# Performance work log

Hardware: AMD Instinct MI355X
Metric: run time of the kernel (lower is better)

The kernel has to match this reference:

```python
import jax, jax.numpy as jnp
import numpy as np

NEG_BIG = -9.0e15  # matches -9000000000000000.0 in the torch source


def setup_inputs() -> dict:
    key = jax.random.key(0)
    k1, k2 = jax.random.split(key)
    N, D, L = 8192, 128, 2
    features = jax.random.normal(k1, (N, D), dtype=jnp.float32)
    adj_lst = jax.random.randint(k2, (L, N, N), 0, 2, dtype=jnp.int32)
    return {"features": features, "adj_lst": adj_lst}


def reference(features, adj_lst):
    # features: [N, D] float; adj_lst: [L, N, N] int (0/1)
    n_node = features.shape[0]
    for i in range(adj_lst.shape[0]):  # small fixed number of propagation steps
        adj = adj_lst[i]
        mask = adj > 0
        # raw_weight = ones -> masked logits are 1.0 on edges, -9e15 elsewhere
        logits = jnp.where(mask, jnp.float32(1.0), jnp.float32(NEG_BIG))
        attention = jax.nn.softmax(logits, axis=1)          # [N, N] row-stochastic
        prop_fea = attention @ features                     # [N, D] neighbor mean
        adj_num = jnp.sum(adj, axis=1)                      # degree per node
        adj_mask = (adj_num > 0).astype(features.dtype)[:, None]  # [N, 1]
        features = adj_mask * prop_fea + (1.0 - adj_mask) * features
    return features
```

## Files before the change

### kernel.cpp

```cpp
#include <hip/hip_runtime.h>
#include <hip/hip_bf16.h>

typedef __bf16 bf16x8 __attribute__((ext_vector_type(8)));
typedef float f32x4 __attribute__((ext_vector_type(4)));
typedef float f32x16 __attribute__((ext_vector_type(16)));
typedef int int4v __attribute__((ext_vector_type(4)));
typedef unsigned int uint4v __attribute__((ext_vector_type(4)));
typedef unsigned short u16x8 __attribute__((ext_vector_type(8)));

#define N_NODES 8192
#define D_FEAT 128

__device__ __forceinline__ bf16x8 unpack_byte(unsigned dword, int sh) {
  unsigned P = ((dword >> sh) & 0xFFu) * 0x8001u;
  uint4v c;
  c[0] = (P & 0x10001u) * 0x3F80u;
  c[1] = ((P >> 2) & 0x10001u) * 0x3F80u;
  c[2] = ((P >> 4) & 0x10001u) * 0x3F80u;
  c[3] = ((P >> 6) & 0x10001u) * 0x3F80u;
  return __builtin_bit_cast(bf16x8, c);
}

__device__ __forceinline__ void bpk32_store(const float* __restrict__ src,
                                            unsigned short* __restrict__ Bpk,
                                            int W) {
  const int kk = W >> 8;
  const int ng = (W >> 6) & 3;
  const int l = W & 63;
  const int d = ng * 32 + (l & 31);
  const int p0 = kk * 16 + (l >> 5) * 8;
  const int n0 = (p0 >> 8) * 256 + ((p0 >> 3) & 7) * 32 + ((p0 >> 6) & 3);
  u16x8 pk;
#pragma unroll
  for (int e = 0; e < 8; ++e) {
    __bf16 v = (__bf16)src[(long)(n0 + 4 * e) * D_FEAT + d];
    pk[e] = __builtin_bit_cast(unsigned short, v);
  }
  *(u16x8*)(Bpk + (long)W * 8) = pk;
}

__global__ __launch_bounds__(256) void pack_all_kernel(
    const int* __restrict__ adj, unsigned long long* __restrict__ bits64,
    int* __restrict__ deg, const float* __restrict__ fsrc,
    unsigned short* __restrict__ Bpk) {
  const int bx = blockIdx.x;
  const int t = threadIdx.x;

  if (bx < 512) {
    bpk32_store(fsrc, Bpk, bx * 256 + t);
    return;
  }

  const int row = bx - 512;
  const int w = t >> 6;
  const int lane = t & 63;
  const int4v* p = (const int4v*)(adj + ((long)row << 13));
  int4v v[8];
#pragma unroll
  for (int j = 0; j < 8; ++j) v[j] = p[j * 256 + t];

  unsigned long long* brow = bits64 + ((long)row << 7);
  int cnt = 0;
#pragma unroll
  for (int j = 0; j < 8; ++j) {
    unsigned long long b0 = __ballot(v[j][0] != 0);
    unsigned long long b1 = __ballot(v[j][1] != 0);
    unsigned long long b2 = __ballot(v[j][2] != 0);
    unsigned long long b3 = __ballot(v[j][3] != 0);
    cnt += __popcll(b0) + __popcll(b1) + __popcll(b2) + __popcll(b3);
    unsigned long long bsel = b0;
    if (lane == 1) bsel = b1;
    if (lane == 2) bsel = b2;
    if (lane == 3) bsel = b3;
    if (lane < 4) brow[16 * j + 4 * w + lane] = bsel;
  }
  __shared__ int red[4];
  if (lane == 0) red[w] = cnt;
  __syncthreads();
  if (t == 0) deg[row] = red[0] + red[1] + red[2] + red[3];
}

__global__ __launch_bounds__(256) void bpk_build32_kernel(
    const float* __restrict__ src, unsigned short* __restrict__ Bpk) {
  bpk32_store(src, Bpk, blockIdx.x * 256 + threadIdx.x);
}

__device__ __forceinline__ void layer_body32(
    int rowblk, int nthalf,
    const unsigned* __restrict__ bits, const int* __restrict__ deg,
    const unsigned short* __restrict__ Bpk,
    const float* fin, float* fout,
    f32x4 (*red)[2][2][4][64]) {
  const int tid = threadIdx.x;
  const int lane = tid & 63;
  const int w = tid >> 6;
  const int ntl = w & 1;
  const int kh = w >> 1;
  const int l31 = lane & 31;
  const int lh = lane >> 5;
  const int m0 = rowblk * 64;
  const int ng = nthalf * 2 + ntl;
  const int shA = lh * 8;
  const int shB = shA + 16;

  const uint4v* ap0 = (const uint4v*)(bits + ((long)(m0 + l31) << 8)) + kh * 16;
  const uint4v* ap1 =
      (const uint4v*)(bits + ((long)(m0 + 32 + l31) << 8)) + kh * 16;
  const bf16x8* bp = (const bf16x8*)Bpk + ((long)kh << 15) + ng * 64 + lane;

  f32x16 acc0 = {0.f, 0.f, 0.f, 0.f, 0.f, 0.f, 0.f, 0.f,
                 0.f, 0.f, 0.f, 0.f, 0.f, 0.f, 0.f, 0.f};
  f32x16 acc1 = {0.f, 0.f, 0.f, 0.f, 0.f, 0.f, 0.f, 0.f,
                 0.f, 0.f, 0.f, 0.f, 0.f, 0.f, 0.f, 0.f};

#pragma unroll 2
  for (int kg = 0; kg < 16; ++kg) {
    uint4v a0 = ap0[kg];
    uint4v a1 = ap1[kg];
#pragma unroll
    for (int s = 0; s < 8; ++s) {
      bf16x8 bv = *bp;
      bp += 256;
      const int sh = (s & 1) ? shB : shA;
      acc0 = __builtin_amdgcn_mfma_f32_32x32x16_bf16(
          unpack_byte(a0[s >> 1], sh), bv, acc0, 0, 0, 0);
      acc1 = __builtin_amdgcn_mfma_f32_32x32x16_bf16(
          unpack_byte(a1[s >> 1], sh), bv, acc1, 0, 0, 0);
    }
  }

  if (kh) {
#define STORE_CHUNK(c)                                                       \
  red[kh - 1][ntl][0][c][lane] = __builtin_shufflevector(                    \
      acc0, acc0, 4 * (c), 4 * (c) + 1, 4 * (c) + 2, 4 * (c) + 3);           \
  red[kh - 1][ntl][1][c][lane] = __builtin_shufflevector(                    \
      acc1, acc1, 4 * (c), 4 * (c) + 1, 4 * (c) + 2, 4 * (c) + 3);
    STORE_CHUNK(0)
    STORE_CHUNK(1)
    STORE_CHUNK(2)
    STORE_CHUNK(3)
#undef STORE_CHUNK
  }
  __syncthreads();
  if (kh) return;

#pragma unroll
  for (int q = 0; q < 3; ++q) {
#pragma unroll
    for (int c = 0; c < 4; ++c) {
      f32x4 r0 = red[q][ntl][0][c][lane];
      f32x4 r1 = red[q][ntl][1][c][lane];
#pragma unroll
      for (int k = 0; k < 4; ++k) {
        acc0[4 * c + k] += r0[k];
        acc1[4 * c + k] += r1[k];
      }
    }
  }

#pragma unroll
  for (int mt = 0; mt < 2; ++mt) {
#pragma unroll
    for (int r = 0; r < 16; ++r) {
      const int row = m0 + mt * 32 + (r & 3) + 8 * (r >> 2) + 4 * lh;
      const int dg = deg[row];
      const float a = mt ? acc1[r] : acc0[r];
      const long off = (long)row * D_FEAT + ng * 32 + l31;
      fout[off] = dg > 0 ? a * (1.0f / (float)dg) : fin[off];
    }
  }
}

__global__ __launch_bounds__(512, 2) void layer32_kernel(
    const unsigned* __restrict__ bits, const int* __restrict__ deg,
    const unsigned short* __restrict__ Bpk, const float* fin, float* fout) {
  __shared__ __align__(16) f32x4 red[3][2][2][4][64];
  layer_body32(blockIdx.x >> 1, blockIdx.x & 1, bits, deg, Bpk, fin, fout,
               red);
}

__global__ __launch_bounds__(256) void transpose_cast_kernel(
    const float* __restrict__ src, unsigned short* __restrict__ dst) {
  __shared__ float tile[64][129];
  const int t = threadIdx.x;
  const int nbase = blockIdx.x * 64;
#pragma unroll
  for (int i = 0; i < 32; ++i) {
    int idx = t + i * 256;
    int nl = idx >> 7;
    int d = idx & 127;
    tile[nl][d] = src[(long)(nbase + nl) * D_FEAT + d];
  }
  __syncthreads();
#pragma unroll
  for (int i = 0; i < 32; ++i) {
    int idx = t + i * 256;
    int d = idx >> 6;
    int nl = idx & 63;
    __bf16 b = (__bf16)tile[nl][d];
    dst[(long)d * N_NODES + nbase + nl] = __builtin_bit_cast(unsigned short, b);
  }
}

__global__ __launch_bounds__(512) void layer_kernel_direct(
    const int* __restrict__ adj, const unsigned short* __restrict__ BT,
    const float* __restrict__ fin, float* __restrict__ fout) {
  const int tid = threadIdx.x;
  const int lane = tid & 63;
  const int w = tid >> 6;
  const int m0 = blockIdx.x * 32 + (w >> 2) * 16;
  const int n0 = (w & 3) * 32;
  const int lr = lane & 15;
  const int kc = lane >> 4;

  const int4v* ap = (const int4v*)(adj + (long)(m0 + lr) * N_NODES + kc * 8);
  const bf16x8* bp0 = (const bf16x8*)(BT + (long)(n0 + lr) * N_NODES + kc * 8);
  const bf16x8* bp1 =
      (const bf16x8*)(BT + (long)(n0 + 16 + lr) * N_NODES + kc * 8);

  f32x4 acc0 = {0.f, 0.f, 0.f, 0.f};
  f32x4 acc1 = {0.f, 0.f, 0.f, 0.f};
  int degv = 0;

#pragma unroll 4
  for (int k = 0; k < N_NODES; k += 32) {
    int4v alo = ap[0];
    int4v ahi = ap[1];
    bf16x8 b0 = bp0[0];
    bf16x8 b1 = bp1[0];
    ap += 8;
    bp0 += 4;
    bp1 += 4;
    unsigned short u[8];
    u[0] = alo[0] ? 0x3F80 : 0;
    u[1] = alo[1] ? 0x3F80 : 0;
    u[2] = alo[2] ? 0x3F80 : 0;
    u[3] = alo[3] ? 0x3F80 : 0;
    u[4] = ahi[0] ? 0x3F80 : 0;
    u[5] = ahi[1] ? 0x3F80 : 0;
    u[6] = ahi[2] ? 0x3F80 : 0;
    u[7] = ahi[3] ? 0x3F80 : 0;
    degv += alo[0] + alo[1] + alo[2] + alo[3] + ahi[0] + ahi[1] + ahi[2] +
            ahi[3];
    bf16x8 a;
    memcpy(&a, u, 16);
    acc0 = __builtin_amdgcn_mfma_f32_16x16x32_bf16(a, b0, acc0, 0, 0, 0);
    acc1 = __builtin_amdgcn_mfma_f32_16x16x32_bf16(a, b1, acc1, 0, 0, 0);
  }

  degv += __shfl_xor(degv, 16);
  degv += __shfl_xor(degv, 32);
  int dgv[4];
#pragma unroll
  for (int j = 0; j < 4; ++j) dgv[j] = __shfl(degv, kc * 4 + j);

#pragma unroll
  for (int t = 0; t < 2; ++t) {
    const f32x4 acc = t ? acc1 : acc0;
    const int col = n0 + t * 16 + lr;
#pragma unroll
    for (int j = 0; j < 4; ++j) {
      const long off = (long)(m0 + kc * 4 + j) * D_FEAT + col;
      fout[off] = dgv[j] > 0 ? acc[j] * (1.0f / (float)dgv[j]) : fin[off];
    }
  }
}

extern "C" void kernel_launch(void* const* d_in, const int* in_sizes, int n_in,
                              void* d_out, int out_size, void* d_ws,
                              size_t ws_size, hipStream_t stream) {
  const float* features = (const float*)d_in[0];
  const int* adj = (const int*)d_in[1];
  float* out = (float*)d_out;
  const long NN = (long)N_NODES * N_NODES;

  const size_t BITS_BYTES = 2ul * N_NODES * 128 * 8;
  const size_t BPK_BYTES = (size_t)D_FEAT * N_NODES * 2;
  const size_t NEED = BITS_BYTES + 65536 + BPK_BYTES;

  if (ws_size >= NEED) {
    unsigned long long* bits64 = (unsigned long long*)d_ws;
    int* degw = (int*)((char*)d_ws + BITS_BYTES);
    unsigned short* Bpk = (unsigned short*)((char*)d_ws + BITS_BYTES + 65536);
    const unsigned* bits32 = (const unsigned*)d_ws;

    pack_all_kernel<<<2 * N_NODES + 512, 256, 0, stream>>>(adj, bits64, degw,
                                                           features, Bpk);
    layer32_kernel<<<256, 512, 0, stream>>>(bits32, degw, Bpk, features, out);
    bpk_build32_kernel<<<512, 256, 0, stream>>>(out, Bpk);
    layer32_kernel<<<256, 512, 0, stream>>>(bits32 + (size_t)N_NODES * 256,
                                            degw + N_NODES, Bpk, out, out);
  } else {
    unsigned short* BTw = (unsigned short*)d_ws;
    transpose_cast_kernel<<<N_NODES / 64, 256, 0, stream>>>(features, BTw);
    layer_kernel_direct<<<N_NODES / 32, 512, 0, stream>>>(adj, BTw, features,
                                                          out);
    transpose_cast_kernel<<<N_NODES / 64, 256, 0, stream>>>(out, BTw);
    layer_kernel_direct<<<N_NODES / 32, 512, 0, stream>>>(adj + NN, BTw, out,
                                                          out);
  }
}
```

Baseline: 175.5 us.

## Persistent adjacency packing with nontemporal loads and 2x2 MFMA tiles per wave

The packing kernel now launches 2048 row blocks that each loop over 8 rows, and it reads the adjacency matrix with nontemporal loads. This cuts block launch overhead and avoids polluting the cache with the large int32 adjacency stream. The layer kernel now has each wave compute a 2x2 set of 32x32 MFMA tiles over one-eighth of K, so each B fragment is reused across two A tiles and each unpacked A across two B tiles. The cross-wave K reduction becomes a two-stage tree through LDS, which adds registers (four accumulators), extra syncs and more LDS.

```diff
diff --git a/kernel.cpp b/kernel.cpp
--- a/kernel.cpp
+++ b/kernel.cpp
@@ -51,38 +51,64 @@
     return;
   }
 
-  const int row = bx - 512;
+  const int bxp = bx - 512;
   const int w = t >> 6;
   const int lane = t & 63;
-  const int4v* p = (const int4v*)(adj + ((long)row << 13));
-  int4v v[8];
-#pragma unroll
-  for (int j = 0; j < 8; ++j) v[j] = p[j * 256 + t];
-
-  unsigned long long* brow = bits64 + ((long)row << 7);
-  int cnt = 0;
-#pragma unroll
-  for (int j = 0; j < 8; ++j) {
-    unsigned long long b0 = __ballot(v[j][0] != 0);
-    unsigned long long b1 = __ballot(v[j][1] != 0);
-    unsigned long long b2 = __ballot(v[j][2] != 0);
-    unsigned long long b3 = __ballot(v[j][3] != 0);
-    cnt += __popcll(b0) + __popcll(b1) + __popcll(b2) + __popcll(b3);
-    unsigned long long bsel = b0;
-    if (lane == 1) bsel = b1;
-    if (lane == 2) bsel = b2;
-    if (lane == 3) bsel = b3;
-    if (lane < 4) brow[16 * j + 4 * w + lane] = bsel;
-  }
-  __shared__ int red[4];
-  if (lane == 0) red[w] = cnt;
-  __syncthreads();
-  if (t == 0) deg[row] = red[0] + red[1] + red[2] + red[3];
+  __shared__ int red[2][4];
+
+  for (int it = 0; it < 8; ++it) {
+    const int row = bxp + it * 2048;
+    const int4v* p = (const int4v*)(adj + ((long)row << 13));
+    int4v v[8];
+#pragma unroll
+    for (int j = 0; j < 8; ++j)
+      v[j] = __builtin_nontemporal_load(p + j * 256 + t);
+
+    unsigned long long* brow = bits64 + ((long)row << 7);
+    int cnt = 0;
+#pragma unroll
+    for (int j = 0; j < 8; ++j) {
+      unsigned long long b0 = __ballot(v[j][0] != 0);
+      unsigned long long b1 = __ballot(v[j][1] != 0);
+      unsigned long long b2 = __ballot(v[j][2] != 0);
+      unsigned long long b3 = __ballot(v[j][3] != 0);
+      cnt += __popcll(b0) + __popcll(b1) + __popcll(b2) + __popcll(b3);
+      unsigned long long bsel = b0;
+      if (lane == 1) bsel = b1;
+      if (lane == 2) bsel = b2;
+      if (lane == 3) bsel = b3;
+      if (lane < 4) brow[16 * j + 4 * w + lane] = bsel;
+    }
+    if (lane == 0) red[it & 1][w] = cnt;
+    __syncthreads();
+    if (t == 0)
+      deg[row] =
+          red[it & 1][0] + red[it & 1][1] + red[it & 1][2] + red[it & 1][3];
+  }
 }
 
 __global__ __launch_bounds__(256) void bpk_build32_kernel(
     const float* __restrict__ src, unsigned short* __restrict__ Bpk) {
   bpk32_store(src, Bpk, blockIdx.x * 256 + threadIdx.x);
+}
+
+__device__ __forceinline__ void st_acc(f32x4 (*red)[16][64], int slot, int A,
+                                       int lane, f32x16 v) {
+  red[slot][A * 4 + 0][lane] = __builtin_shufflevector(v, v, 0, 1, 2, 3);
+  red[slot][A * 4 + 1][lane] = __builtin_shufflevector(v, v, 4, 5, 6, 7);
+  red[slot][A * 4 + 2][lane] = __builtin_shufflevector(v, v, 8, 9, 10, 11);
+  red[slot][A * 4 + 3][lane] = __builtin_shufflevector(v, v, 12, 13, 14, 15);
+}
+__device__ __forceinline__ void ld_acc(f32x4 (*red)[16][64], int slot, int A,
+                                       int lane, f32x16* v) {
+#pragma unroll
+  for (int c = 0; c < 4; ++c) {
+    f32x4 r = red[slot][A * 4 + c][lane];
+    (*v)[4 * c + 0] += r[0];
+    (*v)[4 * c + 1] += r[1];
+    (*v)[4 * c + 2] += r[2];
+    (*v)[4 * c + 3] += r[3];
+  }
 }
 
 __device__ __forceinline__ void layer_body32(
@@ -90,83 +116,90 @@
     const unsigned* __restrict__ bits, const int* __restrict__ deg,
     const unsigned short* __restrict__ Bpk,
     const float* fin, float* fout,
-    f32x4 (*red)[2][2][4][64]) {
+    f32x4 (*red)[16][64]) {
   const int tid = threadIdx.x;
   const int lane = tid & 63;
   const int w = tid >> 6;
-  const int ntl = w & 1;
-  const int kh = w >> 1;
   const int l31 = lane & 31;
   const int lh = lane >> 5;
   const int m0 = rowblk * 64;
-  const int ng = nthalf * 2 + ntl;
+  const int ng0 = nthalf * 2;
   const int shA = lh * 8;
-  const int shB = shA + 16;
-
-  const uint4v* ap0 = (const uint4v*)(bits + ((long)(m0 + l31) << 8)) + kh * 16;
+
+  const uint4v* ap0 = (const uint4v*)(bits + ((long)(m0 + l31) << 8)) + w * 8;
   const uint4v* ap1 =
-      (const uint4v*)(bits + ((long)(m0 + 32 + l31) << 8)) + kh * 16;
-  const bf16x8* bp = (const bf16x8*)Bpk + ((long)kh << 15) + ng * 64 + lane;
-
-  f32x16 acc0 = {0.f, 0.f, 0.f, 0.f, 0.f, 0.f, 0.f, 0.f,
-                 0.f, 0.f, 0.f, 0.f, 0.f, 0.f, 0.f, 0.f};
-  f32x16 acc1 = {0.f, 0.f, 0.f, 0.f, 0.f, 0.f, 0.f, 0.f,
-                 0.f, 0.f, 0.f, 0.f, 0.f, 0.f, 0.f, 0.f};
+      (const uint4v*)(bits + ((long)(m0 + 32 + l31) << 8)) + w * 8;
+  const bf16x8* bp = (const bf16x8*)Bpk + ((long)w << 14) + ng0 * 64 + lane;
+
+  f32x16 acc00 = {0.f, 0.f, 0.f, 0.f, 0.f, 0.f, 0.f, 0.f,
+                  0.f, 0.f, 0.f, 0.f, 0.f, 0.f, 0.f, 0.f};
+  f32x16 acc01 = acc00, acc10 = acc00, acc11 = acc00;
 
 #pragma unroll 2
-  for (int kg = 0; kg < 16; ++kg) {
+  for (int kg = 0; kg < 8; ++kg) {
     uint4v a0 = ap0[kg];
     uint4v a1 = ap1[kg];
 #pragma unroll
     for (int s = 0; s < 8; ++s) {
-      bf16x8 bv = *bp;
+      bf16x8 bv0 = bp[0];
+      bf16x8 bv1 = bp[64];
       bp += 256;
-      const int sh = (s & 1) ? shB : shA;
-      acc0 = __builtin_amdgcn_mfma_f32_32x32x16_bf16(
-          unpack_byte(a0[s >> 1], sh), bv, acc0, 0, 0, 0);
-      acc1 = __builtin_amdgcn_mfma_f32_32x32x16_bf16(
-          unpack_byte(a1[s >> 1], sh), bv, acc1, 0, 0, 0);
+      const int sh = shA + (s & 1) * 16;
+      bf16x8 af0 = unpack_byte(a0[s >> 1], sh);
+      bf16x8 af1 = unpack_byte(a1[s >> 1], sh);
+      acc00 = __builtin_amdgcn_mfma_f32_32x32x16_bf16(af0, bv0, acc00, 0, 0, 0);
+      acc10 = __builtin_amdgcn_mfma_f32_32x32x16_bf16(af1, bv0, acc10, 0, 0, 0);
+      acc01 = __builtin_amdgcn_mfma_f32_32x32x16_bf16(af0, bv1, acc01, 0, 0, 0);
+      acc11 = __builtin_amdgcn_mfma_f32_32x32x16_bf16(af1, bv1, acc11, 0, 0, 0);
     }
   }
 
-  if (kh) {
-#define STORE_CHUNK(c)                                                       \
-  red[kh - 1][ntl][0][c][lane] = __builtin_shufflevector(                    \
-      acc0, acc0, 4 * (c), 4 * (c) + 1, 4 * (c) + 2, 4 * (c) + 3);           \
-  red[kh - 1][ntl][1][c][lane] = __builtin_shufflevector(                    \
-      acc1, acc1, 4 * (c), 4 * (c) + 1, 4 * (c) + 2, 4 * (c) + 3);
-    STORE_CHUNK(0)
-    STORE_CHUNK(1)
-    STORE_CHUNK(2)
-    STORE_CHUNK(3)
-#undef STORE_CHUNK
+  if (w >= 4) {
+    st_acc(red, w - 4, 0, lane, acc00);
+    st_acc(red, w - 4, 1, lane, acc01);
+    st_acc(red, w - 4, 2, lane, acc10);
+    st_acc(red, w - 4, 3, lane, acc11);
   }
   __syncthreads();
-  if (kh) return;
-
-#pragma unroll
-  for (int q = 0; q < 3; ++q) {
-#pragma unroll
-    for (int c = 0; c < 4; ++c) {
-      f32x4 r0 = red[q][ntl][0][c][lane];
-      f32x4 r1 = red[q][ntl][1][c][lane];
-#pragma unroll
-      for (int k = 0; k < 4; ++k) {
-        acc0[4 * c + k] += r0[k];
-        acc1[4 * c + k] += r1[k];
+  if (w < 4) {
+    ld_acc(red, w, 0, lane, &acc00);
+    ld_acc(red, w, 1, lane, &acc01);
+    ld_acc(red, w, 2, lane, &acc10);
+    ld_acc(red, w, 3, lane, &acc11);
+  }
+  __syncthreads();
+  if (w >= 1 && w < 4) {
+    st_acc(red, w, 0, lane, acc00);
+    st_acc(red, w, 1, lane, acc01);
+    st_acc(red, w, 2, lane, acc10);
+    st_acc(red, w, 3, lane, acc11);
+  }
+  __syncthreads();
+  if (w != 0) return;
+#pragma unroll
+  for (int q = 1; q < 4; ++q) {
+    ld_acc(red, q, 0, lane, &acc00);
+    ld_acc(red, q, 1, lane, &acc01);
+    ld_acc(red, q, 2, lane, &acc10);
+    ld_acc(red, q, 3, lane, &acc11);
+  }
+
+#pragma unroll
+  for (int mt = 0; mt < 2; ++mt) {
+#pragma unroll
+    for (int nn = 0; nn < 2; ++nn) {
+#pragma unroll
+      for (int r = 0; r < 16; ++r) {
+        const int row = m0 + mt * 32 + (r & 3) + 8 * (r >> 2) + 4 * lh;
+        const int dg = deg[row];
+        float a;
+        if (mt == 0 && nn == 0) a = acc00[r];
+        else if (mt == 0 && nn == 1) a = acc01[r];
+        else if (mt == 1 && nn == 0) a = acc10[r];
+        else a = acc11[r];
+        const long off = (long)row * D_FEAT + (ng0 + nn) * 32 + l31;
+        fout[off] = dg > 0 ? a * (1.0f / (float)dg) : fin[off];
       }
-    }
-  }
-
-#pragma unroll
-  for (int mt = 0; mt < 2; ++mt) {
-#pragma unroll
-    for (int r = 0; r < 16; ++r) {
-      const int row = m0 + mt * 32 + (r & 3) + 8 * (r >> 2) + 4 * lh;
-      const int dg = deg[row];
-      const float a = mt ? acc1[r] : acc0[r];
-      const long off = (long)row * D_FEAT + ng * 32 + l31;
-      fout[off] = dg > 0 ? a * (1.0f / (float)dg) : fin[off];
     }
   }
 }
@@ -174,7 +207,7 @@
 __global__ __launch_bounds__(512, 2) void layer32_kernel(
     const unsigned* __restrict__ bits, const int* __restrict__ deg,
     const unsigned short* __restrict__ Bpk, const float* fin, float* fout) {
-  __shared__ __align__(16) f32x4 red[3][2][2][4][64];
+  __shared__ __align__(16) f32x4 red[4][16][64];
   layer_body32(blockIdx.x >> 1, blockIdx.x & 1, bits, deg, Bpk, fin, fout,
                red);
 }
@@ -284,8 +317,8 @@
     unsigned short* Bpk = (unsigned short*)((char*)d_ws + BITS_BYTES + 65536);
     const unsigned* bits32 = (const unsigned*)d_ws;
 
-    pack_all_kernel<<<2 * N_NODES + 512, 256, 0, stream>>>(adj, bits64, degw,
-                                                           features, Bpk);
+    pack_all_kernel<<<2048 + 512, 256, 0, stream>>>(adj, bits64, degw,
+                                                    features, Bpk);
     layer32_kernel<<<256, 512, 0, stream>>>(bits32, degw, Bpk, features, out);
     bpk_build32_kernel<<<512, 256, 0, stream>>>(out, Bpk);
     layer32_kernel<<<256, 512, 0, stream>>>(bits32 + (size_t)N_NODES * 256,
```

New measurement: 183.1 us. +4.4%, slower.

## Fuse adjacency bit-packing and degree counting into the layer GEMM kernel

Applied to the files above, without the earlier changes.

Removes the separate pack kernel that converted the whole int32 adjacency into a global bitmask and degree array. Each layer kernel now streams its own 32 adjacency rows, ballots them into a double-buffered shared-memory bitmask and counts degrees. The bf16 MFMA GEMM on the previous chunk runs while the next chunks are prefetched, so the adjacency read overlaps with compute. The cost is one block per 32 rows, only 256 blocks, with a barrier per chunk. Bandwidth saturation now depends on the register prefetch depth rather than on massive block parallelism.

```diff
diff --git a/kernel.cpp b/kernel.cpp
--- a/kernel.cpp
+++ b/kernel.cpp
@@ -10,6 +10,7 @@
 
 #define N_NODES 8192
 #define D_FEAT 128
+
 
 __device__ __forceinline__ bf16x8 unpack_byte(unsigned dword, int sh) {
   unsigned P = ((dword >> sh) & 0xFFu) * 0x8001u;
@@ -39,144 +40,144 @@
   *(u16x8*)(Bpk + (long)W * 8) = pk;
 }
 
-__global__ __launch_bounds__(256) void pack_all_kernel(
-    const int* __restrict__ adj, unsigned long long* __restrict__ bits64,
-    int* __restrict__ deg, const float* __restrict__ fsrc,
-    unsigned short* __restrict__ Bpk) {
-  const int bx = blockIdx.x;
-  const int t = threadIdx.x;
-
-  if (bx < 512) {
-    bpk32_store(fsrc, Bpk, bx * 256 + t);
-    return;
-  }
-
-  const int row = bx - 512;
-  const int w = t >> 6;
-  const int lane = t & 63;
-  const int4v* p = (const int4v*)(adj + ((long)row << 13));
-  int4v v[8];
-#pragma unroll
-  for (int j = 0; j < 8; ++j) v[j] = p[j * 256 + t];
-
-  unsigned long long* brow = bits64 + ((long)row << 7);
-  int cnt = 0;
-#pragma unroll
-  for (int j = 0; j < 8; ++j) {
-    unsigned long long b0 = __ballot(v[j][0] != 0);
-    unsigned long long b1 = __ballot(v[j][1] != 0);
-    unsigned long long b2 = __ballot(v[j][2] != 0);
-    unsigned long long b3 = __ballot(v[j][3] != 0);
-    cnt += __popcll(b0) + __popcll(b1) + __popcll(b2) + __popcll(b3);
-    unsigned long long bsel = b0;
-    if (lane == 1) bsel = b1;
-    if (lane == 2) bsel = b2;
-    if (lane == 3) bsel = b3;
-    if (lane < 4) brow[16 * j + 4 * w + lane] = bsel;
-  }
-  __shared__ int red[4];
-  if (lane == 0) red[w] = cnt;
-  __syncthreads();
-  if (t == 0) deg[row] = red[0] + red[1] + red[2] + red[3];
-}
-
 __global__ __launch_bounds__(256) void bpk_build32_kernel(
     const float* __restrict__ src, unsigned short* __restrict__ Bpk) {
   bpk32_store(src, Bpk, blockIdx.x * 256 + threadIdx.x);
 }
 
-__device__ __forceinline__ void layer_body32(
-    int rowblk, int nthalf,
-    const unsigned* __restrict__ bits, const int* __restrict__ deg,
-    const unsigned short* __restrict__ Bpk,
-    const float* fin, float* fout,
-    f32x4 (*red)[2][2][4][64]) {
+__global__ __launch_bounds__(512, 2) void fused_layer_kernel(
+    const int* __restrict__ adj, const unsigned short* __restrict__ Bpk,
+    const float* __restrict__ fin, float* __restrict__ fout) {
+  __shared__ unsigned bitsL[2][320];
+  __shared__ int degL[32];
+  __shared__ __align__(16) f32x4 red[4][4][64];
+
   const int tid = threadIdx.x;
   const int lane = tid & 63;
   const int w = tid >> 6;
-  const int ntl = w & 1;
-  const int kh = w >> 1;
+  const int ng = w & 3;
+  const int kh2 = w >> 2;
   const int l31 = lane & 31;
   const int lh = lane >> 5;
-  const int m0 = rowblk * 64;
-  const int ng = nthalf * 2 + ntl;
-  const int shA = lh * 8;
-  const int shB = shA + 16;
-
-  const uint4v* ap0 = (const uint4v*)(bits + ((long)(m0 + l31) << 8)) + kh * 16;
-  const uint4v* ap1 =
-      (const uint4v*)(bits + ((long)(m0 + 32 + l31) << 8)) + kh * 16;
-  const bf16x8* bp = (const bf16x8*)Bpk + ((long)kh << 15) + ng * 64 + lane;
-
-  f32x16 acc0 = {0.f, 0.f, 0.f, 0.f, 0.f, 0.f, 0.f, 0.f,
-                 0.f, 0.f, 0.f, 0.f, 0.f, 0.f, 0.f, 0.f};
-  f32x16 acc1 = {0.f, 0.f, 0.f, 0.f, 0.f, 0.f, 0.f, 0.f,
-                 0.f, 0.f, 0.f, 0.f, 0.f, 0.f, 0.f, 0.f};
-
-#pragma unroll 2
-  for (int kg = 0; kg < 16; ++kg) {
-    uint4v a0 = ap0[kg];
-    uint4v a1 = ap1[kg];
-#pragma unroll
-    for (int s = 0; s < 8; ++s) {
-      bf16x8 bv = *bp;
-      bp += 256;
-      const int sh = (s & 1) ? shB : shA;
-      acc0 = __builtin_amdgcn_mfma_f32_32x32x16_bf16(
-          unpack_byte(a0[s >> 1], sh), bv, acc0, 0, 0, 0);
-      acc1 = __builtin_amdgcn_mfma_f32_32x32x16_bf16(
-          unpack_byte(a1[s >> 1], sh), bv, acc1, 0, 0, 0);
-    }
-  }
-
-  if (kh) {
-#define STORE_CHUNK(c)                                                       \
-  red[kh - 1][ntl][0][c][lane] = __builtin_shufflevector(                    \
-      acc0, acc0, 4 * (c), 4 * (c) + 1, 4 * (c) + 2, 4 * (c) + 3);           \
-  red[kh - 1][ntl][1][c][lane] = __builtin_shufflevector(                    \
-      acc1, acc1, 4 * (c), 4 * (c) + 1, 4 * (c) + 2, 4 * (c) + 3);
-    STORE_CHUNK(0)
-    STORE_CHUNK(1)
-    STORE_CHUNK(2)
-    STORE_CHUNK(3)
-#undef STORE_CHUNK
-  }
+  const int lh8 = lh * 8;
+  const int m0 = blockIdx.x * 32;
+
+  const int4v* aB0 = (const int4v*)(adj + ((long)(m0 + w) << 13)) + lane;
+  const int4v* aB1 = (const int4v*)(adj + ((long)(m0 + 8 + w) << 13)) + lane;
+  const int4v* aB2 = (const int4v*)(adj + ((long)(m0 + 16 + w) << 13)) + lane;
+  const int4v* aB3 = (const int4v*)(adj + ((long)(m0 + 24 + w) << 13)) + lane;
+
+  int cnt0 = 0, cnt1 = 0, cnt2 = 0, cnt3 = 0;
+
+#define DO_BALLOT(R0, R1, R2, R3, BUF)                                       \
+  {                                                                          \
+    const int e_ = lane >> 1;                                                \
+    _Pragma("unroll") for (int i = 0; i < 4; ++i) {                          \
+      int4v vv = (i == 0) ? (R0) : (i == 1) ? (R1) : (i == 2) ? (R2) : (R3); \
+      unsigned long long b0 = __ballot(vv[0] != 0);                          \
+      unsigned long long b1 = __ballot(vv[1] != 0);                          \
+      unsigned long long b2 = __ballot(vv[2] != 0);                          \
+      unsigned long long b3 = __ballot(vv[3] != 0);                          \
+      int pc = __popcll(b0) + __popcll(b1) + __popcll(b2) + __popcll(b3);    \
+      if (i == 0) cnt0 += pc;                                                \
+      if (i == 1) cnt1 += pc;                                                \
+      if (i == 2) cnt2 += pc;                                                \
+      if (i == 3) cnt3 += pc;                                                \
+      unsigned long long bsel = b0;                                          \
+      if (e_ == 1) bsel = b1;                                                \
+      if (e_ == 2) bsel = b2;                                                \
+      if (e_ == 3) bsel = b3;                                                \
+      unsigned dv = (lane & 1) ? (unsigned)(bsel >> 32) : (unsigned)bsel;    \
+      if (lane < 8) bitsL[BUF][(i * 8 + w) * 10 + lane] = dv;                \
+    }                                                                        \
+  }
+
+  f32x16 acc = {0.f, 0.f, 0.f, 0.f, 0.f, 0.f, 0.f, 0.f,
+                0.f, 0.f, 0.f, 0.f, 0.f, 0.f, 0.f, 0.f};
+
+#define DO_GEMM(C, BUF)                                                      \
+  {                                                                          \
+    const bf16x8* bp = (const bf16x8*)Bpk +                                  \
+                       (((long)((C)*16 + kh2 * 8)) << 8) + ng * 64 + lane;   \
+    bf16x8 bv0 = bp[0], bv1 = bp[256], bv2 = bp[512], bv3 = bp[768];         \
+    bf16x8 bv4 = bp[1024], bv5 = bp[1280], bv6 = bp[1536], bv7 = bp[1792];   \
+    const unsigned* bl = &bitsL[BUF][l31 * 10 + kh2 * 4];                    \
+    unsigned q0 = bl[0], q1 = bl[1], q2 = bl[2], q3 = bl[3];                 \
+    acc = __builtin_amdgcn_mfma_f32_32x32x16_bf16(unpack_byte(q0, lh8),      \
+                                                  bv0, acc, 0, 0, 0);        \
+    acc = __builtin_amdgcn_mfma_f32_32x32x16_bf16(unpack_byte(q0, lh8 + 16), \
+                                                  bv1, acc, 0, 0, 0);        \
+    acc = __builtin_amdgcn_mfma_f32_32x32x16_bf16(unpack_byte(q1, lh8),      \
+                                                  bv2, acc, 0, 0, 0);        \
+    acc = __builtin_amdgcn_mfma_f32_32x32x16_bf16(unpack_byte(q1, lh8 + 16), \
+                                                  bv3, acc, 0, 0, 0);        \
+    acc = __builtin_amdgcn_mfma_f32_32x32x16_bf16(unpack_byte(q2, lh8),      \
+                                                  bv4, acc, 0, 0, 0);        \
+    acc = __builtin_amdgcn_mfma_f32_32x32x16_bf16(unpack_byte(q2, lh8 + 16), \
+                                                  bv5, acc, 0, 0, 0);        \
+    acc = __builtin_amdgcn_mfma_f32_32x32x16_bf16(unpack_byte(q3, lh8),      \
+                                                  bv6, acc, 0, 0, 0);        \
+    acc = __builtin_amdgcn_mfma_f32_32x32x16_bf16(unpack_byte(q3, lh8 + 16), \
+                                                  bv7, acc, 0, 0, 0);        \
+  }
+
+  int4v avA0 = aB0[0], avA1 = aB1[0], avA2 = aB2[0], avA3 = aB3[0];
+  int4v avB0 = aB0[64], avB1 = aB1[64], avB2 = aB2[64], avB3 = aB3[64];
+  DO_BALLOT(avA0, avA1, avA2, avA3, 0)
   __syncthreads();
-  if (kh) return;
-
-#pragma unroll
-  for (int q = 0; q < 3; ++q) {
-#pragma unroll
-    for (int c = 0; c < 4; ++c) {
-      f32x4 r0 = red[q][ntl][0][c][lane];
-      f32x4 r1 = red[q][ntl][1][c][lane];
-#pragma unroll
-      for (int k = 0; k < 4; ++k) {
-        acc0[4 * c + k] += r0[k];
-        acc1[4 * c + k] += r1[k];
-      }
-    }
-  }
-
-#pragma unroll
-  for (int mt = 0; mt < 2; ++mt) {
-#pragma unroll
-    for (int r = 0; r < 16; ++r) {
-      const int row = m0 + mt * 32 + (r & 3) + 8 * (r >> 2) + 4 * lh;
-      const int dg = deg[row];
-      const float a = mt ? acc1[r] : acc0[r];
-      const long off = (long)row * D_FEAT + ng * 32 + l31;
-      fout[off] = dg > 0 ? a * (1.0f / (float)dg) : fin[off];
-    }
-  }
-}
-
-__global__ __launch_bounds__(512, 2) void layer32_kernel(
-    const unsigned* __restrict__ bits, const int* __restrict__ deg,
-    const unsigned short* __restrict__ Bpk, const float* fin, float* fout) {
-  __shared__ __align__(16) f32x4 red[3][2][2][4][64];
-  layer_body32(blockIdx.x >> 1, blockIdx.x & 1, bits, deg, Bpk, fin, fout,
-               red);
+
+#define BODY(C, CUR0, CUR1, CUR2, CUR3, OTH0, OTH1, OTH2, OTH3)              \
+  {                                                                          \
+    if ((C) + 2 < 32) {                                                      \
+      CUR0 = aB0[((C) + 2) * 64];                                            \
+      CUR1 = aB1[((C) + 2) * 64];                                            \
+      CUR2 = aB2[((C) + 2) * 64];                                            \
+      CUR3 = aB3[((C) + 2) * 64];                                            \
+    }                                                                        \
+    if ((C) + 1 < 32) DO_BALLOT(OTH0, OTH1, OTH2, OTH3, ((C) + 1) & 1)       \
+    DO_GEMM((C), (C)&1)                                                      \
+    __syncthreads();                                                         \
+  }
+
+  for (int c = 0; c < 32; c += 2) {
+    BODY(c, avA0, avA1, avA2, avA3, avB0, avB1, avB2, avB3)
+    BODY(c + 1, avB0, avB1, avB2, avB3, avA0, avA1, avA2, avA3)
+  }
+#undef BODY
+#undef DO_GEMM
+#undef DO_BALLOT
+
+  if (lane == 0) {
+    degL[w] = cnt0;
+    degL[8 + w] = cnt1;
+    degL[16 + w] = cnt2;
+    degL[24 + w] = cnt3;
+  }
+
+  if (kh2) {
+#define ST4(c)                                                               \
+  red[ng][c][lane] = __builtin_shufflevector(acc, acc, 4 * (c), 4 * (c) + 1, \
+                                             4 * (c) + 2, 4 * (c) + 3);
+    ST4(0) ST4(1) ST4(2) ST4(3)
+#undef ST4
+  }
+  __syncthreads();
+  if (kh2) return;
+#pragma unroll
+  for (int c = 0; c < 4; ++c) {
+    f32x4 r = red[ng][c][lane];
+#pragma unroll
+    for (int k = 0; k < 4; ++k) acc[4 * c + k] += r[k];
+  }
+
+#pragma unroll
+  for (int r = 0; r < 16; ++r) {
+    const int row32 = (r & 3) + 8 * (r >> 2) + 4 * lh;
+    const int row = m0 + row32;
+    const int dg = degL[row32];
+    const long off = (long)row * D_FEAT + ng * 32 + l31;
+    fout[off] = dg > 0 ? acc[r] * (1.0f / (float)dg) : fin[off];
+  }
 }
 
 __global__ __launch_bounds__(256) void transpose_cast_kernel(
@@ -274,22 +275,16 @@
   float* out = (float*)d_out;
   const long NN = (long)N_NODES * N_NODES;
 
-  const size_t BITS_BYTES = 2ul * N_NODES * 128 * 8;
   const size_t BPK_BYTES = (size_t)D_FEAT * N_NODES * 2;
-  const size_t NEED = BITS_BYTES + 65536 + BPK_BYTES;
+  const size_t NEED = BPK_BYTES + 256;
 
   if (ws_size >= NEED) {
-    unsigned long long* bits64 = (unsigned long long*)d_ws;
-    int* degw = (int*)((char*)d_ws + BITS_BYTES);
-    unsigned short* Bpk = (unsigned short*)((char*)d_ws + BITS_BYTES + 65536);
-    const unsigned* bits32 = (const unsigned*)d_ws;
-
-    pack_all_kernel<<<2 * N_NODES + 512, 256, 0, stream>>>(adj, bits64, degw,
-                                                           features, Bpk);
-    layer32_kernel<<<256, 512, 0, stream>>>(bits32, degw, Bpk, features, out);
+    unsigned short* Bpk = (unsigned short*)d_ws;
+
+    bpk_build32_kernel<<<512, 256, 0, stream>>>(features, Bpk);
+    fused_layer_kernel<<<256, 512, 0, stream>>>(adj, Bpk, features, out);
     bpk_build32_kernel<<<512, 256, 0, stream>>>(out, Bpk);
-    layer32_kernel<<<256, 512, 0, stream>>>(bits32 + (size_t)N_NODES * 256,
-                                            degw + N_NODES, Bpk, out, out);
+    fused_layer_kernel<<<256, 512, 0, stream>>>(adj + NN, Bpk, out, out);
   } else {
     unsigned short* BTw = (unsigned short*)d_ws;
     transpose_cast_kernel<<<N_NODES / 64, 256, 0, stream>>>(features, BTw);
```

After: 157.6 us. -10.2%, faster.
